# Kernel tuning notes

Hardware: AMD Instinct MI355X
Metric: run time of the kernel (lower is better)

The kernel has to match this reference:

```python
import jax, jax.numpy as jnp
import numpy as np

H = 96
NH = 4
HD = H // NH
SPARSITY = 0.5
LN_EPS = 1e-5


def _lstm_layer(xs, w_ih, w_hh, b_ih, b_hh):
    # xs: [B, T, I]; PyTorch gate order i, f, g, o
    B = xs.shape[0]
    Hd = w_hh.shape[1]
    def step(carry, x_t):
        h, c = carry
        gates = x_t @ w_ih.T + h @ w_hh.T + b_ih + b_hh  # [B, 4H]
        i, f, g, o = jnp.split(gates, 4, axis=-1)
        i = jax.nn.sigmoid(i); f = jax.nn.sigmoid(f)
        g = jnp.tanh(g); o = jax.nn.sigmoid(o)
        c = f * c + i * g
        h = o * jnp.tanh(c)
        return (h, c), h
    h0 = jnp.zeros((B, Hd), xs.dtype)
    c0 = jnp.zeros((B, Hd), xs.dtype)
    _, hs = jax.lax.scan(step, (h0, c0), xs.transpose(1, 0, 2))  # [T, B, H]
    return hs.transpose(1, 0, 2)


def _layer_norm(x, w, b):
    mu = jnp.mean(x, axis=-1, keepdims=True)
    var = jnp.mean((x - mu) ** 2, axis=-1, keepdims=True)
    return (x - mu) * jax.lax.rsqrt(var + LN_EPS) * w + b


def _split_heads(x, B, T):
    return x.reshape(B, T, NH, HD).transpose(0, 2, 1, 3)  # [B, H, T, d]


def _sparse_attention(x, qw, kw, vw, ow):
    B, T, _ = x.shape
    q = _split_heads(x @ qw.T, B, T)
    k = _split_heads(x @ kw.T, B, T)
    v = _split_heads(x @ vw.T, B, T)
    scores = jnp.einsum('bhtd,bhsd->bhts', q, k) / np.sqrt(HD).astype(np.float32)
    num_keep = int(T * SPARSITY)
    topv, _ = jax.lax.top_k(scores, num_keep)
    kth = topv[..., -1:]  # threshold == k-th largest (equiv to topk+scatter mask for distinct values)
    scores = jnp.where(scores >= kth, scores, -jnp.inf)
    attn = jax.nn.softmax(scores, axis=-1)  # dropout is identity in eval
    out = jnp.einsum('bhts,bhsd->bhtd', attn, v)
    out = out.transpose(0, 2, 1, 3).reshape(B, T, H)
    return out @ ow.T


def _mha(x, in_w, in_b, out_w, out_b):
    B, T, _ = x.shape
    qkv = x @ in_w.T + in_b  # [B, T, 3H]
    q, k, v = jnp.split(qkv, 3, axis=-1)
    q = _split_heads(q, B, T); k = _split_heads(k, B, T); v = _split_heads(v, B, T)
    scores = jnp.einsum('bhtd,bhsd->bhts', q, k) / np.sqrt(HD).astype(np.float32)
    attn = jax.nn.softmax(scores, axis=-1)
    out = jnp.einsum('bhts,bhsd->bhtd', attn, v)
    out = out.transpose(0, 2, 1, 3).reshape(B, T, H)
    return out @ out_w.T + out_b


def _encoder_layer(x, in_w, in_b, out_w, out_b, l1_w, l1_b, l2_w, l2_b, ln1_w, ln1_b, ln2_w, ln2_b):
    # PyTorch TransformerEncoderLayer, post-norm, ReLU, eval (no dropout)
    x = _layer_norm(x + _mha(x, in_w, in_b, out_w, out_b), ln1_w, ln1_b)
    ff = jax.nn.relu(x @ l1_w.T + l1_b) @ l2_w.T + l2_b
    return _layer_norm(x + ff, ln2_w, ln2_b)


def setup_inputs() -> dict:
    key = jax.random.key(0)
    ks = iter(jax.random.split(key, 40))
    B, T, I = 16, 1024, 64
    FF = 2 * H
    def rnd(shape, scale=0.05):
        return (jax.random.normal(next(ks), shape, dtype=jnp.float32) * scale)
    inp = {
        'x': jax.random.normal(next(ks), (B, T, I), dtype=jnp.float32),
        'w_ih0': rnd((4 * H, I)), 'w_hh0': rnd((4 * H, H)),
        'b_ih0': rnd((4 * H,)), 'b_hh0': rnd((4 * H,)),
        'w_ih1': rnd((4 * H, H)), 'w_hh1': rnd((4 * H, H)),
        'b_ih1': rnd((4 * H,)), 'b_hh1': rnd((4 * H,)),
        'qw': rnd((H, H)), 'kw': rnd((H, H)), 'vw': rnd((H, H)), 'ow': rnd((H, H)),
        'enc_in_w': rnd((2, 3 * H, H)), 'enc_in_b': rnd((2, 3 * H)),
        'enc_out_w': rnd((2, H, H)), 'enc_out_b': rnd((2, H)),
        'enc_l1_w': rnd((2, FF, H)), 'enc_l1_b': rnd((2, FF)),
        'enc_l2_w': rnd((2, H, FF)), 'enc_l2_b': rnd((2, H)),
        'enc_ln1_w': jnp.ones((2, H), jnp.float32), 'enc_ln1_b': jnp.zeros((2, H), jnp.float32),
        'enc_ln2_w': jnp.ones((2, H), jnp.float32), 'enc_ln2_b': jnp.zeros((2, H), jnp.float32),
        'fc_w': rnd((1, H)), 'fc_b': rnd((1,)),
    }
    return inp


def reference(x, w_ih0, w_hh0, b_ih0, b_hh0, w_ih1, w_hh1, b_ih1, b_hh1,
              qw, kw, vw, ow,
              enc_in_w, enc_in_b, enc_out_w, enc_out_b,
              enc_l1_w, enc_l1_b, enc_l2_w, enc_l2_b,
              enc_ln1_w, enc_ln1_b, enc_ln2_w, enc_ln2_b,
              fc_w, fc_b):
    h = _lstm_layer(x, w_ih0, w_hh0, b_ih0, b_hh0)
    h = _lstm_layer(h, w_ih1, w_hh1, b_ih1, b_hh1)
    h = _sparse_attention(h, qw, kw, vw, ow)
    for i in range(2):
        h = _encoder_layer(h, enc_in_w[i], enc_in_b[i], enc_out_w[i], enc_out_b[i],
                           enc_l1_w[i], enc_l1_b[i], enc_l2_w[i], enc_l2_b[i],
                           enc_ln1_w[i], enc_ln1_b[i], enc_ln2_w[i], enc_ln2_b[i])
    return h[:, -1, :] @ fc_w.T + fc_b  # [B, 1]
```

## Files before the change

kernel.cpp:

```cpp
#include <hip/hip_runtime.h>
#include <cstdint>
#include <cmath>

#define T_SEQ 1024
#define BATCH 16
#define HID 96
#define G4 384
#define QKV_LD 288
#define HDIM 24
#define KKEEP 512
#define SCALE 0.20412414523193154f
#define L2E 1.4426950408889634f

typedef _Float16 half2v __attribute__((ext_vector_type(2)));

__device__ __forceinline__ float wred_sum(float v){
#pragma unroll
  for (int o=32;o;o>>=1) v += __shfl_xor(v,o,64);
  return v;
}
__device__ __forceinline__ float wred_max(float v){
#pragma unroll
  for (int o=32;o;o>>=1) v = fmaxf(v,__shfl_xor(v,o,64));
  return v;
}
__device__ __forceinline__ int wred_sumi(int v){
#pragma unroll
  for (int o=32;o;o>>=1) v += __shfl_xor(v,o,64);
  return v;
}
__device__ __forceinline__ unsigned fmono(float f){
  unsigned u = __float_as_uint(f);
  return (u & 0x80000000u) ? ~u : (u | 0x80000000u);
}
__device__ __forceinline__ float sigf(float x){
  return __builtin_amdgcn_rcpf(1.f + __builtin_amdgcn_exp2f(-L2E*x));
}
__device__ __forceinline__ float tanhf2(float x){
  return fmaf(-2.f, __builtin_amdgcn_rcpf(1.f + __builtin_amdgcn_exp2f((2.f*L2E)*x)), 1.f);
}
template<int CTRL>
__device__ __forceinline__ float dpp_add_f(float v){
  int s = __builtin_amdgcn_update_dpp(0, __float_as_int(v), CTRL, 0xF, 0xF, true);
  return v + __int_as_float(s);
}
__device__ __forceinline__ float dpp_red4(float v){
  v = dpp_add_f<0xB1>(v);
  v = dpp_add_f<0x4E>(v);
  return v;
}
#if __has_builtin(__builtin_amdgcn_fdot2)
__device__ __forceinline__ float fdot2(half2v a, half2v b, float c){
  return __builtin_amdgcn_fdot2(a, b, c, false);
}
#else
__device__ __forceinline__ float fdot2(half2v a, half2v b, float c){
  return fmaf((float)a[0], (float)b[0], fmaf((float)a[1], (float)b[1], c));
}
#endif

__global__ __launch_bounds__(256)
void gemm_kernel(const float* __restrict__ A, const float* __restrict__ W,
                 const float* __restrict__ b1, const float* __restrict__ b2,
                 float* __restrict__ C, int M, int N, int K,
                 int ldc, int coff, int relu)
{
  __shared__ float As[16][68];
  __shared__ float Ws[16][68];
  const int tid = threadIdx.x;
  const int tx = tid & 15, ty = tid >> 4;
  const int m0 = blockIdx.y * 64, n0 = blockIdx.x * 64;
  const int lrow = tid >> 2, lcol = (tid & 3) * 4;
  float acc[4][4] = {};
  for (int k0 = 0; k0 < K; k0 += 16) {
    float4 a = {0,0,0,0}, w = {0,0,0,0};
    int gm = m0 + lrow;
    if (gm < M) a = *(const float4*)(A + (size_t)gm*K + k0 + lcol);
    int gn = n0 + lrow;
    if (gn < N) w = *(const float4*)(W + (size_t)gn*K + k0 + lcol);
    __syncthreads();
    As[lcol+0][lrow]=a.x; As[lcol+1][lrow]=a.y; As[lcol+2][lrow]=a.z; As[lcol+3][lrow]=a.w;
    Ws[lcol+0][lrow]=w.x; Ws[lcol+1][lrow]=w.y; Ws[lcol+2][lrow]=w.z; Ws[lcol+3][lrow]=w.w;
    __syncthreads();
#pragma unroll
    for (int kk=0;kk<16;++kk){
      const float4 av = *(const float4*)&As[kk][ty*4];
      const float4 wv = *(const float4*)&Ws[kk][tx*4];
      float a_[4]={av.x,av.y,av.z,av.w};
      float w_[4]={wv.x,wv.y,wv.z,wv.w};
#pragma unroll
      for (int i=0;i<4;++i)
#pragma unroll
        for (int j=0;j<4;++j) acc[i][j] += a_[i]*w_[j];
    }
  }
#pragma unroll
  for (int i=0;i<4;++i){
    int gm = m0 + ty*4 + i;
    if (gm >= M) continue;
#pragma unroll
    for (int j=0;j<4;++j){
      int gn = n0 + tx*4 + j;
      if (gn >= N) continue;
      float v = acc[i][j];
      if (b1) v += b1[gn];
      if (b2) v += b2[gn];
      if (relu) v = fmaxf(v, 0.f);
      C[(size_t)gm*ldc + coff + gn] = v;
    }
  }
}

__global__ __launch_bounds__(384)
void lstm_kernel(const float* __restrict__ pre, const float* __restrict__ w_hh,
                 float* __restrict__ hout)
{
  const int b = blockIdx.x;
  const int tid = threadIdx.x;
  const int q = tid & 3, j = tid >> 2;
  half2v w[4][12];
#pragma unroll
  for (int g=0; g<4; ++g){
    const float* wp = w_hh + (size_t)(g*96 + j)*96 + q*24;
#pragma unroll
    for (int k=0;k<12;++k){
      half2v t; t[0] = (_Float16)wp[2*k]; t[1] = (_Float16)wp[2*k+1];
      w[g][k] = t;
    }
  }
  __shared__ _Float16 h_lds[96];
  float c = 0.f;
  if (tid < 96) h_lds[tid] = (_Float16)0.f;
  __syncthreads();

  const float* prow = pre + (size_t)b*T_SEQ*G4 + q*96 + j;
  float* hrow = hout + (size_t)b*T_SEQ*HID;
  float pf[4];
#pragma unroll
  for (int i=0;i<4;++i) pf[i] = prow[(size_t)i*G4];

  for (int tb=0; tb<T_SEQ; tb+=4){
#pragma unroll
    for (int u=0; u<4; ++u){
      const int t = tb + u;
      const float pcur = pf[u];
      int tn = t + 4; if (tn > T_SEQ-1) tn = T_SEQ-1;
      pf[u] = prow[(size_t)tn*G4];
      const uint4 a0 = *(const uint4*)(h_lds + q*24);
      const uint4 a1 = *(const uint4*)(h_lds + q*24 + 8);
      const uint4 a2 = *(const uint4*)(h_lds + q*24 + 16);
      half2v h2[12];
      h2[0]=__builtin_bit_cast(half2v, a0.x); h2[1]=__builtin_bit_cast(half2v, a0.y);
      h2[2]=__builtin_bit_cast(half2v, a0.z); h2[3]=__builtin_bit_cast(half2v, a0.w);
      h2[4]=__builtin_bit_cast(half2v, a1.x); h2[5]=__builtin_bit_cast(half2v, a1.y);
      h2[6]=__builtin_bit_cast(half2v, a1.z); h2[7]=__builtin_bit_cast(half2v, a1.w);
      h2[8]=__builtin_bit_cast(half2v, a2.x); h2[9]=__builtin_bit_cast(half2v, a2.y);
      h2[10]=__builtin_bit_cast(half2v, a2.z); h2[11]=__builtin_bit_cast(half2v, a2.w);

      float sA0=0.f,sA1=0.f,sA2=0.f,sA3=0.f;
      float sB0=0.f,sB1=0.f,sB2=0.f,sB3=0.f;
#pragma unroll
      for (int k=0;k<12;k+=2){
        sA0 = fdot2(w[0][k], h2[k], sA0);  sB0 = fdot2(w[0][k+1], h2[k+1], sB0);
        sA1 = fdot2(w[1][k], h2[k], sA1);  sB1 = fdot2(w[1][k+1], h2[k+1], sB1);
        sA2 = fdot2(w[2][k], h2[k], sA2);  sB2 = fdot2(w[2][k+1], h2[k+1], sB2);
        sA3 = fdot2(w[3][k], h2[k], sA3);  sB3 = fdot2(w[3][k+1], h2[k+1], sB3);
      }
      float s0 = sA0+sB0, s1 = sA1+sB1, s2 = sA2+sB2, s3 = sA3+sB3;
      s0 += (q==0) ? pcur : 0.f;
      s1 += (q==1) ? pcur : 0.f;
      s2 += (q==2) ? pcur : 0.f;
      s3 += (q==3) ? pcur : 0.f;
      s0 = dpp_red4(s0);
      s1 = dpp_red4(s1);
      s2 = dpp_red4(s2);
      s3 = dpp_red4(s3);
      const float iv = sigf(s0), fv = sigf(s1);
      const float gv = tanhf2(s2), ov = sigf(s3);
      c = fmaf(fv, c, iv*gv);
      const float hv = ov * tanhf2(c);
      if (q == 0){
        h_lds[j] = (_Float16)hv;
        hrow[t*HID + j] = hv;
      }
      __syncthreads();
    }
  }
}

__global__ __launch_bounds__(512)
void attn_kernel(const float* __restrict__ qkv, float* __restrict__ out, int sparse)
{
  __shared__ float kl[24][260];
  const int tid = threadIdx.x;
  const int wave = tid >> 6, lane = tid & 63;
  const int bh = blockIdx.x >> 7;
  const int b = bh >> 2, h = bh & 3;
  const int tq = ((blockIdx.x & 127) << 3) + wave;
  const size_t base = (size_t)b * T_SEQ;
  const int hoff = h * HDIM;
  float q[24];
  {
    const float* qp = qkv + (base + tq)*QKV_LD + hoff;
#pragma unroll
    for (int d4=0; d4<6; ++d4){
      float4 t = *(const float4*)(qp + d4*4);
      q[d4*4]=t.x; q[d4*4+1]=t.y; q[d4*4+2]=t.z; q[d4*4+3]=t.w;
    }
  }
  float sc[16];
  for (int c=0;c<4;++c){
    __syncthreads();
#pragma unroll
    for (int rep=0;rep<3;++rep){
      int p = rep*512 + tid;
      int sl = p/6, d4 = p - sl*6;
      const float4 kv = *(const float4*)(qkv + (base + (c<<8) + sl)*QKV_LD + 96 + hoff + d4*4);
      kl[d4*4+0][sl]=kv.x; kl[d4*4+1][sl]=kv.y; kl[d4*4+2][sl]=kv.z; kl[d4*4+3][sl]=kv.w;
    }
    __syncthreads();
    float a0=0.f,a1=0.f,a2=0.f,a3=0.f;
#pragma unroll
    for (int d=0; d<24; ++d){
      const float4 kd = *(const float4*)&kl[d][lane*4];
      a0 += q[d]*kd.x; a1 += q[d]*kd.y; a2 += q[d]*kd.z; a3 += q[d]*kd.w;
    }
    sc[c*4+0]=a0*SCALE; sc[c*4+1]=a1*SCALE; sc[c*4+2]=a2*SCALE; sc[c*4+3]=a3*SCALE;
  }
  float m_loc = sc[0];
#pragma unroll
  for (int i=1;i<16;++i) m_loc = fmaxf(m_loc, sc[i]);
  const float m = wred_max(m_loc);
  float sum_loc = 0.f;
  if (sparse){
    unsigned u[16];
#pragma unroll
    for (int i=0;i<16;++i) u[i] = fmono(sc[i]);
    unsigned prefix = 0;
    for (int bit=31; bit>=0; --bit){
      unsigned test = prefix | (1u<<bit);
      int cnt = 0;
#pragma unroll
      for (int i=0;i<16;++i) cnt += (u[i] >= test) ? 1 : 0;
      cnt = wred_sumi(cnt);
      if (cnt >= KKEEP) prefix = test;
    }
#pragma unroll
    for (int i=0;i<16;++i){
      float e = (u[i] >= prefix) ? __expf(sc[i]-m) : 0.f;
      sc[i] = e; sum_loc += e;
    }
  } else {
#pragma unroll
    for (int i=0;i<16;++i){
      float e = __expf(sc[i]-m);
      sc[i] = e; sum_loc += e;
    }
  }
  const float inv = 1.f / wred_sum(sum_loc);
#pragma unroll
  for (int i=0;i<16;++i) sc[i] *= inv;
  float acc[24] = {};
  for (int c=0;c<4;++c){
    __syncthreads();
#pragma unroll
    for (int rep=0;rep<3;++rep){
      int p = rep*512 + tid;
      int sl = p/6, d4 = p - sl*6;
      const float4 vv = *(const float4*)(qkv + (base + (c<<8) + sl)*QKV_LD + 192 + hoff + d4*4);
      kl[d4*4+0][sl]=vv.x; kl[d4*4+1][sl]=vv.y; kl[d4*4+2][sl]=vv.z; kl[d4*4+3][sl]=vv.w;
    }
    __syncthreads();
    const float w0=sc[c*4], w1=sc[c*4+1], w2=sc[c*4+2], w3=sc[c*4+3];
#pragma unroll
    for (int d=0; d<24; ++d){
      const float4 vd = *(const float4*)&kl[d][lane*4];
      acc[d] += w0*vd.x + w1*vd.y + w2*vd.z + w3*vd.w;
    }
  }
#pragma unroll
  for (int d=0; d<24; ++d) acc[d] = wred_sum(acc[d]);
  if (lane == 0){
    float* op = out + (base + tq)*HID + hoff;
#pragma unroll
    for (int d4=0; d4<6; ++d4){
      float4 t = {acc[d4*4], acc[d4*4+1], acc[d4*4+2], acc[d4*4+3]};
      *(float4*)(op + d4*4) = t;
    }
  }
}

__global__ __launch_bounds__(64)
void attn_last_kernel(const float* __restrict__ qkv, float* __restrict__ out)
{
  const int bh = blockIdx.x, b = bh>>2, h = bh&3;
  const int lane = threadIdx.x;
  const size_t base = (size_t)b*T_SEQ;
  const int hoff = h*HDIM;
  float q[24];
  {
    const float* qp = qkv + (base + T_SEQ-1)*QKV_LD + hoff;
#pragma unroll
    for (int d4=0; d4<6; ++d4){
      float4 t = *(const float4*)(qp + d4*4);
      q[d4*4]=t.x; q[d4*4+1]=t.y; q[d4*4+2]=t.z; q[d4*4+3]=t.w;
    }
  }
  float sc[16];
#pragma unroll 4
  for (int i=0;i<16;++i){
    const float* kp = qkv + (base + i*64 + lane)*QKV_LD + 96 + hoff;
    float a = 0.f;
#pragma unroll
    for (int d4=0; d4<6; ++d4){
      float4 kv = *(const float4*)(kp + d4*4);
      a += q[d4*4]*kv.x + q[d4*4+1]*kv.y + q[d4*4+2]*kv.z + q[d4*4+3]*kv.w;
    }
    sc[i] = a*SCALE;
  }
  float m_loc = sc[0];
#pragma unroll
  for (int i=1;i<16;++i) m_loc = fmaxf(m_loc, sc[i]);
  const float m = wred_max(m_loc);
  float sum_loc = 0.f;
#pragma unroll
  for (int i=0;i<16;++i){ sc[i] = __expf(sc[i]-m); sum_loc += sc[i]; }
  const float inv = 1.f / wred_sum(sum_loc);
  float acc[24] = {};
#pragma unroll 4
  for (int i=0;i<16;++i){
    const float* vp = qkv + (base + i*64 + lane)*QKV_LD + 192 + hoff;
    const float wgt = sc[i]*inv;
#pragma unroll
    for (int d4=0; d4<6; ++d4){
      float4 vv = *(const float4*)(vp + d4*4);
      acc[d4*4]   += wgt*vv.x; acc[d4*4+1] += wgt*vv.y;
      acc[d4*4+2] += wgt*vv.z; acc[d4*4+3] += wgt*vv.w;
    }
  }
#pragma unroll
  for (int d=0; d<24; ++d) acc[d] = wred_sum(acc[d]);
  if (lane == 0){
    float* op = out + (base + T_SEQ-1)*HID + hoff;
#pragma unroll
    for (int d4=0; d4<6; ++d4){
      float4 t = {acc[d4*4], acc[d4*4+1], acc[d4*4+2], acc[d4*4+3]};
      *(float4*)(op + d4*4) = t;
    }
  }
}

__global__ __launch_bounds__(256)
void resln_kernel(const float* __restrict__ x, const float* __restrict__ y,
                  const float* __restrict__ w, const float* __restrict__ bb,
                  float* __restrict__ out)
{
  const int row = blockIdx.x*4 + (threadIdx.x>>6);
  const int lane = threadIdx.x & 63;
  const float* xr = x + (size_t)row*HID;
  const float* yr = y + (size_t)row*HID;
  float v0 = xr[lane] + yr[lane];
  float v1 = (lane < 32) ? (xr[64+lane] + yr[64+lane]) : 0.f;
  float mu = wred_sum(v0+v1) * (1.f/96.f);
  float d0 = v0-mu, d1 = (lane<32) ? (v1-mu) : 0.f;
  float var = wred_sum(d0*d0 + d1*d1) * (1.f/96.f);
  float rs = rsqrtf(var + 1e-5f);
  float* orow = out + (size_t)row*HID;
  orow[lane] = d0*rs*w[lane] + bb[lane];
  if (lane < 32) orow[64+lane] = d1*rs*w[64+lane] + bb[64+lane];
}

__device__ __forceinline__ float block_sum_192(float v, float* red){
  v = wred_sum(v);
  const int tid = threadIdx.x;
  if ((tid & 63) == 0) red[tid>>6] = v;
  __syncthreads();
  float r = red[0]+red[1]+red[2];
  __syncthreads();
  return r;
}

__global__ __launch_bounds__(192)
void tail_kernel(const float* __restrict__ xin, const float* __restrict__ mha,
                 const float* __restrict__ out_w, const float* __restrict__ out_b,
                 const float* __restrict__ l1_w, const float* __restrict__ l1_b,
                 const float* __restrict__ l2_w, const float* __restrict__ l2_b,
                 const float* __restrict__ ln1w, const float* __restrict__ ln1b,
                 const float* __restrict__ ln2w, const float* __restrict__ ln2b,
                 const float* __restrict__ fcw, const float* __restrict__ fcb,
                 float* __restrict__ outp)
{
  const int b = blockIdx.x, tid = threadIdx.x;
  __shared__ float y[96], f1[192], mrow[96], red[3];
  const size_t row = ((size_t)b*T_SEQ + T_SEQ-1)*HID;
  if (tid < 96) mrow[tid] = mha[row + tid];
  __syncthreads();
  float r = 0.f;
  if (tid < 96){
    float p = out_b[tid];
    const float* wr = out_w + tid*96;
#pragma unroll 4
    for (int d=0; d<96; ++d) p += mrow[d]*wr[d];
    r = xin[row + tid] + p;
  }
  float mu = block_sum_192(tid<96 ? r : 0.f, red) * (1.f/96.f);
  float dv = tid<96 ? r-mu : 0.f;
  float var = block_sum_192(dv*dv, red) * (1.f/96.f);
  float rs = rsqrtf(var + 1e-5f);
  if (tid < 96) y[tid] = dv*rs*ln1w[tid] + ln1b[tid];
  __syncthreads();
  {
    float a = l1_b[tid];
    const float* wr = l1_w + tid*96;
#pragma unroll 4
    for (int d=0; d<96; ++d) a += y[d]*wr[d];
    f1[tid] = fmaxf(a, 0.f);
  }
  __syncthreads();
  float r2 = 0.f;
  if (tid < 96){
    float a = l2_b[tid];
    const float* wr = l2_w + tid*192;
#pragma unroll 4
    for (int d=0; d<192; ++d) a += f1[d]*wr[d];
    r2 = y[tid] + a;
  }
  float mu2 = block_sum_192(tid<96 ? r2 : 0.f, red) * (1.f/96.f);
  float dv2 = tid<96 ? r2-mu2 : 0.f;
  float var2 = block_sum_192(dv2*dv2, red) * (1.f/96.f);
  float rs2 = rsqrtf(var2 + 1e-5f);
  float z = tid<96 ? (dv2*rs2*ln2w[tid] + ln2b[tid]) : 0.f;
  float tot = block_sum_192(tid<96 ? z*fcw[tid] : 0.f, red);
  if (tid == 0) outp[b] = tot + fcb[0];
}

extern "C" void kernel_launch(void* const* d_in, const int* in_sizes, int n_in,
                              void* d_out, int out_size, void* d_ws, size_t ws_size,
                              hipStream_t stream)
{
  const float* x     = (const float*)d_in[0];
  const float* w_ih0 = (const float*)d_in[1];
  const float* w_hh0 = (const float*)d_in[2];
  const float* b_ih0 = (const float*)d_in[3];
  const float* b_hh0 = (const float*)d_in[4];
  const float* w_ih1 = (const float*)d_in[5];
  const float* w_hh1 = (const float*)d_in[6];
  const float* b_ih1 = (const float*)d_in[7];
  const float* b_hh1 = (const float*)d_in[8];
  const float* qw = (const float*)d_in[9];
  const float* kw = (const float*)d_in[10];
  const float* vw = (const float*)d_in[11];
  const float* ow = (const float*)d_in[12];
  const float* enc_in_w  = (const float*)d_in[13];
  const float* enc_in_b  = (const float*)d_in[14];
  const float* enc_out_w = (const float*)d_in[15];
  const float* enc_out_b = (const float*)d_in[16];
  const float* enc_l1_w  = (const float*)d_in[17];
  const float* enc_l1_b  = (const float*)d_in[18];
  const float* enc_l2_w  = (const float*)d_in[19];
  const float* enc_l2_b  = (const float*)d_in[20];
  const float* enc_ln1_w = (const float*)d_in[21];
  const float* enc_ln1_b = (const float*)d_in[22];
  const float* enc_ln2_w = (const float*)d_in[23];
  const float* enc_ln2_b = (const float*)d_in[24];
  const float* fc_w = (const float*)d_in[25];
  const float* fc_b = (const float*)d_in[26];
  float* outp = (float*)d_out;

  float* ws = (float*)d_ws;
  const size_t MT = (size_t)BATCH*T_SEQ;
  float* pre  = ws;
  float* bufA = pre  + MT*G4;
  float* bufB = bufA + MT*HID;
  float* bufC = bufB + MT*HID;

  const int M = (int)MT;
  auto gemm = [&](const float* A, const float* W, const float* bb1, const float* bb2,
                  float* C, int N, int K, int ldc, int coff, int relu){
    dim3 grid((N+63)/64, M/64);
    gemm_kernel<<<grid, dim3(256), 0, stream>>>(A, W, bb1, bb2, C, M, N, K, ldc, coff, relu);
  };

  gemm(x, w_ih0, b_ih0, b_hh0, pre, 384, 64, 384, 0, 0);
  lstm_kernel<<<dim3(BATCH), dim3(384), 0, stream>>>(pre, w_hh0, bufA);
  gemm(bufA, w_ih1, b_ih1, b_hh1, pre, 384, 96, 384, 0, 0);
  lstm_kernel<<<dim3(BATCH), dim3(384), 0, stream>>>(pre, w_hh1, bufB);
  gemm(bufB, qw, nullptr, nullptr, pre, 96, 96, QKV_LD, 0,   0);
  gemm(bufB, kw, nullptr, nullptr, pre, 96, 96, QKV_LD, 96,  0);
  gemm(bufB, vw, nullptr, nullptr, pre, 96, 96, QKV_LD, 192, 0);
  attn_kernel<<<dim3(8192), dim3(512), 0, stream>>>(pre, bufA, 1);
  gemm(bufA, ow, nullptr, nullptr, bufB, 96, 96, 96, 0, 0);
  gemm(bufB, enc_in_w, enc_in_b, nullptr, pre, 288, 96, QKV_LD, 0, 0);
  attn_kernel<<<dim3(8192), dim3(512), 0, stream>>>(pre, bufA, 0);
  gemm(bufA, enc_out_w, enc_out_b, nullptr, bufC, 96, 96, 96, 0, 0);
  resln_kernel<<<dim3(4096), dim3(256), 0, stream>>>(bufB, bufC, enc_ln1_w, enc_ln1_b, bufB);
  gemm(bufB, enc_l1_w, enc_l1_b, nullptr, pre, 192, 96, 192, 0, 1);
  gemm(pre, enc_l2_w, enc_l2_b, nullptr, bufC, 96, 192, 96, 0, 0);
  resln_kernel<<<dim3(4096), dim3(256), 0, stream>>>(bufB, bufC, enc_ln2_w, enc_ln2_b, bufB);
  gemm(bufB, enc_in_w + 288*96, enc_in_b + 288, nullptr, pre, 288, 96, QKV_LD, 0, 0);
  attn_last_kernel<<<dim3(64), dim3(64), 0, stream>>>(pre, bufA);
  tail_kernel<<<dim3(BATCH), dim3(192), 0, stream>>>(
      bufB, bufA,
      enc_out_w + 96*96, enc_out_b + 96,
      enc_l1_w + 192*96, enc_l1_b + 192,
      enc_l2_w + 96*192, enc_l2_b + 96,
      enc_ln1_w + 96, enc_ln1_b + 96,
      enc_ln2_w + 96, enc_ln2_b + 96,
      fc_w, fc_b, outp);
}
```

Before: 2.096 ms.

## Replace FP32 SIMT GEMM with bf16 MFMA kernel and fuse QKV projections

Replaces the scalar FP32 tiled GEMM with a templated bf16 MFMA (16x16x32) kernel that loads the whole K extent into shared memory as bf16 and computes 128x64 tiles per block. It also packs q/k/v weights into one matrix so the three projection GEMMs become a single launch. This reduces the arithmetic cost of the projection and FFN GEMMs, but rounds inputs and weights to bf16, which may lose accuracy. The sparse top-k threshold is sensitive to that rounding.

Result: faster. 1.999 ms (-4.7%).

```diff
diff --git a/kernel.cpp b/kernel.cpp
--- a/kernel.cpp
+++ b/kernel.cpp
@@ -13,6 +13,8 @@
 #define L2E 1.4426950408889634f
 
 typedef _Float16 half2v __attribute__((ext_vector_type(2)));
+typedef __bf16 bf16x8 __attribute__((ext_vector_type(8)));
+typedef float  f32x4v __attribute__((ext_vector_type(4)));
 
 __device__ __forceinline__ float wred_sum(float v){
 #pragma unroll
@@ -58,57 +60,94 @@
   return fmaf((float)a[0], (float)b[0], fmaf((float)a[1], (float)b[1], c));
 }
 #endif
-
+__device__ __forceinline__ unsigned short f2bf(float f){
+  unsigned u = __float_as_uint(f);
+  return (unsigned short)((u + 0x7fffu + ((u>>16)&1u)) >> 16);
+}
+__device__ __forceinline__ f32x4v mfma16(uint4 a, uint4 b, f32x4v c){
+  return __builtin_amdgcn_mfma_f32_16x16x32_bf16(
+      __builtin_bit_cast(bf16x8, a), __builtin_bit_cast(bf16x8, b), c, 0, 0, 0);
+}
+
+template<int K>
 __global__ __launch_bounds__(256)
-void gemm_kernel(const float* __restrict__ A, const float* __restrict__ W,
-                 const float* __restrict__ b1, const float* __restrict__ b2,
-                 float* __restrict__ C, int M, int N, int K,
-                 int ldc, int coff, int relu)
-{
-  __shared__ float As[16][68];
-  __shared__ float Ws[16][68];
+void gemm_mfma(const float* __restrict__ A, const float* __restrict__ W,
+               const float* __restrict__ b1, const float* __restrict__ b2,
+               float* __restrict__ C, int N, int ldc, int coff, int relu)
+{
+  __shared__ unsigned short As[128][K+8];
+  __shared__ unsigned short Ws[64][K+8];
   const int tid = threadIdx.x;
-  const int tx = tid & 15, ty = tid >> 4;
-  const int m0 = blockIdx.y * 64, n0 = blockIdx.x * 64;
-  const int lrow = tid >> 2, lcol = (tid & 3) * 4;
-  float acc[4][4] = {};
-  for (int k0 = 0; k0 < K; k0 += 16) {
-    float4 a = {0,0,0,0}, w = {0,0,0,0};
-    int gm = m0 + lrow;
-    if (gm < M) a = *(const float4*)(A + (size_t)gm*K + k0 + lcol);
-    int gn = n0 + lrow;
-    if (gn < N) w = *(const float4*)(W + (size_t)gn*K + k0 + lcol);
-    __syncthreads();
-    As[lcol+0][lrow]=a.x; As[lcol+1][lrow]=a.y; As[lcol+2][lrow]=a.z; As[lcol+3][lrow]=a.w;
-    Ws[lcol+0][lrow]=w.x; Ws[lcol+1][lrow]=w.y; Ws[lcol+2][lrow]=w.z; Ws[lcol+3][lrow]=w.w;
-    __syncthreads();
-#pragma unroll
-    for (int kk=0;kk<16;++kk){
-      const float4 av = *(const float4*)&As[kk][ty*4];
-      const float4 wv = *(const float4*)&Ws[kk][tx*4];
-      float a_[4]={av.x,av.y,av.z,av.w};
-      float w_[4]={wv.x,wv.y,wv.z,wv.w};
-#pragma unroll
-      for (int i=0;i<4;++i)
-#pragma unroll
-        for (int j=0;j<4;++j) acc[i][j] += a_[i]*w_[j];
-    }
-  }
-#pragma unroll
-  for (int i=0;i<4;++i){
-    int gm = m0 + ty*4 + i;
-    if (gm >= M) continue;
-#pragma unroll
-    for (int j=0;j<4;++j){
-      int gn = n0 + tx*4 + j;
-      if (gn >= N) continue;
-      float v = acc[i][j];
-      if (b1) v += b1[gn];
-      if (b2) v += b2[gn];
-      if (relu) v = fmaxf(v, 0.f);
-      C[(size_t)gm*ldc + coff + gn] = v;
-    }
-  }
+  const int wave = tid >> 6, lane = tid & 63;
+  const int ln = lane & 15, kq = lane >> 4;
+  const int m0 = blockIdx.y * 128, n0 = blockIdx.x * 64;
+
+  for (int idx = tid; idx < 128*(K/4); idx += 256){
+    const int row = idx / (K/4), c4 = idx - row*(K/4);
+    const float4 v = *(const float4*)(A + (size_t)(m0+row)*K + c4*4);
+    ushort4 s = {f2bf(v.x), f2bf(v.y), f2bf(v.z), f2bf(v.w)};
+    *(ushort4*)&As[row][c4*4] = s;
+  }
+  for (int idx = tid; idx < 64*(K/4); idx += 256){
+    const int row = idx / (K/4), c4 = idx - row*(K/4);
+    float4 v = {0,0,0,0};
+    const int gn = n0 + row;
+    if (gn < N) v = *(const float4*)(W + (size_t)gn*K + c4*4);
+    ushort4 s = {f2bf(v.x), f2bf(v.y), f2bf(v.z), f2bf(v.w)};
+    *(ushort4*)&Ws[row][c4*4] = s;
+  }
+  __syncthreads();
+
+  f32x4v acc[2][4];
+#pragma unroll
+  for (int mi=0;mi<2;++mi)
+#pragma unroll
+    for (int ni=0;ni<4;++ni){ f32x4v z = {0.f,0.f,0.f,0.f}; acc[mi][ni] = z; }
+
+#pragma unroll
+  for (int ks=0; ks<K/32; ++ks){
+    uint4 af[2], bf[4];
+#pragma unroll
+    for (int mi=0;mi<2;++mi)
+      af[mi] = *(const uint4*)&As[wave*32 + mi*16 + ln][ks*32 + kq*8];
+#pragma unroll
+    for (int ni=0;ni<4;++ni)
+      bf[ni] = *(const uint4*)&Ws[ni*16 + ln][ks*32 + kq*8];
+#pragma unroll
+    for (int mi=0;mi<2;++mi)
+#pragma unroll
+      for (int ni=0;ni<4;++ni)
+        acc[mi][ni] = mfma16(af[mi], bf[ni], acc[mi][ni]);
+  }
+
+#pragma unroll
+  for (int ni=0;ni<4;++ni){
+    const int gn = n0 + ni*16 + ln;
+    if (gn >= N) continue;
+    float bias = 0.f;
+    if (b1) bias += b1[gn];
+    if (b2) bias += b2[gn];
+#pragma unroll
+    for (int mi=0;mi<2;++mi){
+      const int row = m0 + wave*32 + mi*16 + kq*4;
+#pragma unroll
+      for (int r=0;r<4;++r){
+        float v = acc[mi][ni][r] + bias;
+        if (relu) v = fmaxf(v, 0.f);
+        C[(size_t)(row + r)*ldc + coff + gn] = v;
+      }
+    }
+  }
+}
+
+__global__ __launch_bounds__(256)
+void pack_qkv_kernel(const float* __restrict__ qw, const float* __restrict__ kw,
+                     const float* __restrict__ vw, float* __restrict__ wqkv)
+{
+  const int i = blockIdx.x*256 + threadIdx.x;
+  if (i < 9216)       wqkv[i] = qw[i];
+  else if (i < 18432) wqkv[i] = kw[i-9216];
+  else if (i < 27648) wqkv[i] = vw[i-18432];
 }
 
 __global__ __launch_bounds__(384)
@@ -473,21 +512,26 @@
   float* bufA = pre  + MT*G4;
   float* bufB = bufA + MT*HID;
   float* bufC = bufB + MT*HID;
-
-  const int M = (int)MT;
+  float* wqkv = bufC + MT*HID;
+
   auto gemm = [&](const float* A, const float* W, const float* bb1, const float* bb2,
                   float* C, int N, int K, int ldc, int coff, int relu){
-    dim3 grid((N+63)/64, M/64);
-    gemm_kernel<<<grid, dim3(256), 0, stream>>>(A, W, bb1, bb2, C, M, N, K, ldc, coff, relu);
+    dim3 grid((N+63)/64, 128);
+    if (K == 64)
+      gemm_mfma<64><<<grid, dim3(256), 0, stream>>>(A, W, bb1, bb2, C, N, ldc, coff, relu);
+    else if (K == 96)
+      gemm_mfma<96><<<grid, dim3(256), 0, stream>>>(A, W, bb1, bb2, C, N, ldc, coff, relu);
+    else
+      gemm_mfma<192><<<grid, dim3(256), 0, stream>>>(A, W, bb1, bb2, C, N, ldc, coff, relu);
   };
+
+  pack_qkv_kernel<<<dim3(108), dim3(256), 0, stream>>>(qw, kw, vw, wqkv);
 
   gemm(x, w_ih0, b_ih0, b_hh0, pre, 384, 64, 384, 0, 0);
   lstm_kernel<<<dim3(BATCH), dim3(384), 0, stream>>>(pre, w_hh0, bufA);
   gemm(bufA, w_ih1, b_ih1, b_hh1, pre, 384, 96, 384, 0, 0);
   lstm_kernel<<<dim3(BATCH), dim3(384), 0, stream>>>(pre, w_hh1, bufB);
-  gemm(bufB, qw, nullptr, nullptr, pre, 96, 96, QKV_LD, 0,   0);
-  gemm(bufB, kw, nullptr, nullptr, pre, 96, 96, QKV_LD, 96,  0);
-  gemm(bufB, vw, nullptr, nullptr, pre, 96, 96, QKV_LD, 192, 0);
+  gemm(bufB, wqkv, nullptr, nullptr, pre, 288, 96, QKV_LD, 0, 0);
   attn_kernel<<<dim3(8192), dim3(512), 0, stream>>>(pre, bufA, 1);
   gemm(bufA, ow, nullptr, nullptr, bufB, 96, 96, 96, 0, 0);
   gemm(bufB, enc_in_w, enc_in_b, nullptr, pre, 288, 96, QKV_LD, 0, 0);
```
